# Performance work log

Measured on AMD Instinct MI355X. Metric: run time of the kernel, lower is better.

Reference implementation:

```python
import jax, jax.numpy as jnp
import numpy as np

B, SQ, SKV, D = 4, 4096, 4096, 64

def setup_inputs() -> dict:
    key = jax.random.key(0)
    kq, kv = jax.random.split(key)
    query = jax.random.normal(kq, (B, SQ, D), dtype=jnp.float32)
    value = jax.random.normal(kv, (B, SKV, D), dtype=jnp.float32)
    return {"query": query, "value": value}

def reference(query, value):
    # scores = Q @ V^T  (value acts as both keys and values; no 1/sqrt(d) scaling)
    scores = jnp.einsum('bqd,bkd->bqk', query, value)  # [B, SQ, SKV]
    dist = jax.nn.softmax(scores, axis=-1)
    context = jnp.einsum('bqk,bkd->bqd', dist, value)  # [B, SQ, D]
    return context
```

## Files before the change

kernel.cpp:

```cpp
#include <hip/hip_runtime.h>


#define NB   4
#define SQ   4096
#define SKV  4096
#define DH   64
#define L2E  1.44269504088896340736f

typedef _Float16 half8 __attribute__((ext_vector_type(8)));
typedef _Float16 half4 __attribute__((ext_vector_type(4)));
typedef _Float16 half2v __attribute__((ext_vector_type(2)));
typedef float f32x4 __attribute__((ext_vector_type(4)));
typedef unsigned short u16;

#define MFMA16(a, b, c) __builtin_amdgcn_mfma_f32_16x16x16f16((a), (b), (c), 0, 0, 0)
#define MFMA32(a, b, c) __builtin_amdgcn_mfma_f32_16x16x32_f16((a), (b), (c), 0, 0, 0)

__device__ __forceinline__ u16 f2h(float f) {
  _Float16 h = (_Float16)f;
  return __builtin_bit_cast(u16, h);
}
__device__ __forceinline__ half2v pkrtz(float a, float b) {
  return __builtin_bit_cast(half2v, __builtin_amdgcn_cvt_pkrtz(a, b));
}

__global__ __launch_bounds__(256) void prep_kernel(
    const float* __restrict__ V, u16* __restrict__ vh, u16* __restrict__ vt) {
  __shared__ u16 ldsT[16 * 72];
  int blk = blockIdx.x;
  int b   = blk >> 8;
  int rem = blk & 255;
  int j0  = (rem >> 2) << 6;
  int d0  = (rem & 3) << 4;
  int t   = threadIdx.x;
  int j   = t >> 2;
  int dc  = (t & 3) << 2;

  const float* src = V + ((size_t)(b * SKV) + j0 + j) * DH + d0 + dc;
  float4 v4 = *(const float4*)src;
  u16 h[4] = {f2h(v4.x), f2h(v4.y), f2h(v4.z), f2h(v4.w)};
  unsigned p0 = (unsigned)h[0] | ((unsigned)h[1] << 16);
  unsigned p1 = (unsigned)h[2] | ((unsigned)h[3] << 16);
  size_t go = ((size_t)(b * SKV) + j0 + j) * DH + d0 + dc;
  *(uint2*)(vh + go) = make_uint2(p0, p1);

#pragma unroll
  for (int k = 0; k < 4; ++k) ldsT[(dc + k) * 72 + j] = h[k];
  __syncthreads();

  int dl = t >> 4;
  int jc = (t & 15) << 2;
  u16 tr[4];
#pragma unroll
  for (int k = 0; k < 4; ++k) tr[k] = ldsT[dl * 72 + jc + k];
  unsigned q0 = (unsigned)tr[0] | ((unsigned)tr[1] << 16);
  unsigned q1 = (unsigned)tr[2] | ((unsigned)tr[3] << 16);
  *(uint2*)(vt + ((size_t)(b * DH) + d0 + dl) * SKV + j0 + jc) = make_uint2(q0, q1);
}

__global__ __launch_bounds__(256, 3) void attn_kernel(
    const float* __restrict__ Q,
    const u16* __restrict__ vh,
    const u16* __restrict__ vt,
    u16* __restrict__ po,
    float* __restrict__ pm,
    float* __restrict__ pl,
    int S, int kvLen) {
  __shared__ __align__(16) u16 lds[2][2][64 * 72];

  int blk  = blockIdx.x;
  int tile = blk / S;
  int s    = blk - tile * S;
  int b    = tile >> 5;
  int q0   = (tile & 31) << 7;
  int kv0  = s * kvLen;
  int t    = threadIdx.x;
  int wave = t >> 6;
  int lane = t & 63;
  int col  = lane & 15;
  int quad = lane >> 4;
  int qw   = q0 + (wave << 5);

  half8 qf[2][2];
#pragma unroll
  for (int set = 0; set < 2; ++set) {
#pragma unroll
    for (int kc = 0; kc < 2; ++kc) {
      const float* qp = Q + ((size_t)(b * SQ) + qw + set * 16 + col) * DH +
                        kc * 32 + (quad << 3);
      float4 a0 = *(const float4*)qp;
      float4 a1 = *(const float4*)(qp + 4);
      half8 h;
      h[0] = (_Float16)(a0.x * L2E); h[1] = (_Float16)(a0.y * L2E);
      h[2] = (_Float16)(a0.z * L2E); h[3] = (_Float16)(a0.w * L2E);
      h[4] = (_Float16)(a1.x * L2E); h[5] = (_Float16)(a1.y * L2E);
      h[6] = (_Float16)(a1.z * L2E); h[7] = (_Float16)(a1.w * L2E);
      qf[set][kc] = h;
    }
  }

  f32x4 o[2][4];
  float m_r[2] = {-1e30f, -1e30f};
  float l_r[2] = {0.f, 0.f};
#pragma unroll
  for (int set = 0; set < 2; ++set)
#pragma unroll
    for (int nf = 0; nf < 4; ++nf) o[set][nf] = (f32x4){0.f, 0.f, 0.f, 0.f};

  int sr = t >> 2;
  int sc = (t & 3) << 4;
  const u16* gv  = vh + (size_t)(b * SKV) * DH;
  const u16* gvt = vt + (size_t)(b * DH) * SKV;
  int l0 = sr * 72 + sc;

  {
    size_t g  = (size_t)(kv0 + sr) * DH + sc;
    size_t gt = (size_t)sr * SKV + kv0 + sc;
    *(uint4*)(&lds[0][0][l0])     = *(const uint4*)(gv + g);
    *(uint4*)(&lds[0][0][l0 + 8]) = *(const uint4*)(gv + g + 8);
    *(uint4*)(&lds[0][1][l0])     = *(const uint4*)(gvt + gt);
    *(uint4*)(&lds[0][1][l0 + 8]) = *(const uint4*)(gvt + gt + 8);
  }

  int nIter = kvLen >> 6;
  int cur = 0;
  for (int it = 0; it < nIter; ++it) {
    __syncthreads();

    uint4 a0, a1, c0, c1;
    bool more = (it + 1) < nIter;
    if (more) {
      int j0n = kv0 + ((it + 1) << 6);
      size_t g  = (size_t)(j0n + sr) * DH + sc;
      size_t gt = (size_t)sr * SKV + j0n + sc;
      a0 = *(const uint4*)(gv + g);
      a1 = *(const uint4*)(gv + g + 8);
      c0 = *(const uint4*)(gvt + gt);
      c1 = *(const uint4*)(gvt + gt + 8);
    }

    const u16* sv  = &lds[cur][0][0];
    const u16* svt = &lds[cur][1][0];

    f32x4 sf[2][4];
#pragma unroll
    for (int set = 0; set < 2; ++set)
#pragma unroll
      for (int nf = 0; nf < 4; ++nf) sf[set][nf] = (f32x4){0.f, 0.f, 0.f, 0.f};
#pragma unroll
    for (int nf = 0; nf < 4; ++nf) {
#pragma unroll
      for (int kc = 0; kc < 2; ++kc) {
        half8 av = *(const half8*)(sv + (nf * 16 + col) * 72 + kc * 32 + (quad << 3));
        sf[0][nf] = MFMA32(av, qf[0][kc], sf[0][nf]);
        sf[1][nf] = MFMA32(av, qf[1][kc], sf[1][nf]);
      }
    }

    half4 pf[2][4];
#pragma unroll
    for (int set = 0; set < 2; ++set) {
      float tm = sf[set][0][0];
#pragma unroll
      for (int nf = 0; nf < 4; ++nf)
#pragma unroll
        for (int r = 0; r < 4; ++r) tm = fmaxf(tm, sf[set][nf][r]);
      tm = fmaxf(tm, __shfl_xor(tm, 16, 64));
      tm = fmaxf(tm, __shfl_xor(tm, 32, 64));
      float mn = fmaxf(m_r[set], tm);
      float al = exp2f(m_r[set] - mn);
      m_r[set] = mn;
      float rs = 0.f;
#pragma unroll
      for (int nf = 0; nf < 4; ++nf) {
        float p0 = exp2f(sf[set][nf][0] - mn);
        float p1 = exp2f(sf[set][nf][1] - mn);
        float p2 = exp2f(sf[set][nf][2] - mn);
        float p3 = exp2f(sf[set][nf][3] - mn);
        rs += (p0 + p1) + (p2 + p3);
        half2v lo = pkrtz(p0, p1);
        half2v hi = pkrtz(p2, p3);
        pf[set][nf] = __builtin_shufflevector(lo, hi, 0, 1, 2, 3);
      }
      l_r[set] = l_r[set] * al + rs;
#pragma unroll
      for (int nf = 0; nf < 4; ++nf)
#pragma unroll
        for (int r = 0; r < 4; ++r) o[set][nf][r] *= al;
    }

#pragma unroll
    for (int kc4 = 0; kc4 < 4; ++kc4) {
#pragma unroll
      for (int nf2 = 0; nf2 < 4; ++nf2) {
        half4 avt = *(const half4*)(svt + (nf2 * 16 + col) * 72 + kc4 * 16 + (quad << 2));
        o[0][nf2] = MFMA16(avt, pf[0][kc4], o[0][nf2]);
        o[1][nf2] = MFMA16(avt, pf[1][kc4], o[1][nf2]);
      }
    }

    if (more) {
      u16* dv  = &lds[cur ^ 1][0][0];
      u16* dvt = &lds[cur ^ 1][1][0];
      *(uint4*)(dv + l0)      = a0;
      *(uint4*)(dv + l0 + 8)  = a1;
      *(uint4*)(dvt + l0)     = c0;
      *(uint4*)(dvt + l0 + 8) = c1;
    }
    cur ^= 1;
  }

#pragma unroll
  for (int set = 0; set < 2; ++set) {
    l_r[set] += __shfl_xor(l_r[set], 16, 64);
    l_r[set] += __shfl_xor(l_r[set], 32, 64);
  }
  int pidx = tile * S + s;
  if (quad == 0) {
#pragma unroll
    for (int set = 0; set < 2; ++set) {
      int row = (wave << 5) + set * 16 + col;
      pm[(size_t)pidx * 128 + row] = m_r[set];
      pl[(size_t)pidx * 128 + row] = l_r[set];
    }
  }

  __syncthreads();
  u16* tp = &lds[0][0][0];
#pragma unroll
  for (int set = 0; set < 2; ++set) {
    int q = (wave << 5) + set * 16 + col;
#pragma unroll
    for (int nf2 = 0; nf2 < 4; ++nf2) {
#pragma unroll
      for (int r2 = 0; r2 < 4; r2 += 2) {
        unsigned pk = (unsigned)f2h(o[set][nf2][r2]) |
                      ((unsigned)f2h(o[set][nf2][r2 + 1]) << 16);
        int d = nf2 * 16 + (quad << 2) + r2;
        *(unsigned*)(tp + q * 72 + d) = pk;
      }
    }
  }
  __syncthreads();
  {
    u16* pob = po + (size_t)pidx * 128 * 64;
    int q = t >> 1, hc = (t & 1) << 5;
    uint4 x0 = *(const uint4*)(tp + q * 72 + hc);
    uint4 x1 = *(const uint4*)(tp + q * 72 + hc + 8);
    uint4 x2 = *(const uint4*)(tp + q * 72 + hc + 16);
    uint4 x3 = *(const uint4*)(tp + q * 72 + hc + 24);
    *(uint4*)(pob + q * 64 + hc)      = x0;
    *(uint4*)(pob + q * 64 + hc + 8)  = x1;
    *(uint4*)(pob + q * 64 + hc + 16) = x2;
    *(uint4*)(pob + q * 64 + hc + 24) = x3;
  }
}

__global__ __launch_bounds__(256) void combine_kernel(
    const u16* __restrict__ po,
    const float* __restrict__ pm,
    const float* __restrict__ pl,
    float* __restrict__ out, int S) {
  int t    = threadIdx.x;
  int rowg = blockIdx.x * 32 + (t >> 3);
  int tile = rowg >> 7;
  int row  = rowg & 127;
  int dc   = (t & 7) << 3;

  float mv[8], lv[8];
  float M = -1e30f;
  for (int s = 0; s < S; ++s) {
    mv[s] = pm[(size_t)(tile * S + s) * 128 + row];
    lv[s] = pl[(size_t)(tile * S + s) * 128 + row];
    M = fmaxf(M, mv[s]);
  }
  float L = 0.f, w[8];
  for (int s = 0; s < S; ++s) {
    w[s] = exp2f(mv[s] - M);
    L += lv[s] * w[s];
  }
  float acc[8] = {0.f, 0.f, 0.f, 0.f, 0.f, 0.f, 0.f, 0.f};
  for (int s = 0; s < S; ++s) {
    const u16* p = po + (size_t)(tile * S + s) * 8192 + row * 64 + dc;
    uint4 raw = *(const uint4*)p;
    half8 x = __builtin_bit_cast(half8, raw);
#pragma unroll
    for (int k = 0; k < 8; ++k) acc[k] += w[s] * (float)x[k];
  }
  float invL = 1.0f / L;
  float* op = out + (size_t)rowg * 64 + dc;
  f32x4 o0 = (f32x4){acc[0], acc[1], acc[2], acc[3]};
  f32x4 o1 = (f32x4){acc[4], acc[5], acc[6], acc[7]};
  *(f32x4*)op       = o0 * invL;
  *(f32x4*)(op + 4) = o1 * invL;
}

extern "C" void kernel_launch(void* const* d_in, const int* in_sizes, int n_in,
                              void* d_out, int out_size, void* d_ws, size_t ws_size,
                              hipStream_t stream) {
  const float* Q = (const float*)d_in[0];
  const float* V = (const float*)d_in[1];
  float* out = (float*)d_out;

  const size_t convBytes = (size_t)2 * NB * SKV * DH * 2;
  auto partBytes = [](int S) {
    return (size_t)NB * 32 * S * ((size_t)128 * 64 * 2 + 128 * 8);
  };
  int S = 8;
  while (S > 1 && ws_size < convBytes + partBytes(S)) S >>= 1;
  int kvLen = SKV / S;

  u16* vh = (u16*)d_ws;
  u16* vt = vh + (size_t)NB * SKV * DH;
  u16* po = vt + (size_t)NB * SKV * DH;
  float* pm = (float*)(po + (size_t)NB * 32 * S * 128 * 64);
  float* pl = pm + (size_t)NB * 32 * S * 128;

  prep_kernel<<<NB * 256, 256, 0, stream>>>(V, vh, vt);
  attn_kernel<<<NB * 32 * S, 256, 0, stream>>>(Q, vh, vt, po, pm, pl, S, kvLen);
  combine_kernel<<<NB * SQ / 32, 256, 0, stream>>>(po, pm, pl, out, S);
}
```

Measured before the change: 108.4 us.

## Fuse split-KV combine into attention kernel via last-block atomic counter

Drops the separate combine kernel. Each attention block fences and atomically increments a per-tile counter, and the last block to finish that tile merges the partial outputs, maxes and sums and writes the final result. The counters are zeroed in the prep kernel. This removes one kernel launch and the tail gap between kernels. In exchange, the reduction for each tile runs serially on a single block, and correctness relies on the threadfence and atomic ordering.

```diff
diff --git a/kernel.cpp b/kernel.cpp
--- a/kernel.cpp
+++ b/kernel.cpp
@@ -25,9 +25,11 @@
 }
 
 __global__ __launch_bounds__(256) void prep_kernel(
-    const float* __restrict__ V, u16* __restrict__ vh, u16* __restrict__ vt) {
+    const float* __restrict__ V, u16* __restrict__ vh, u16* __restrict__ vt,
+    unsigned* __restrict__ cnt) {
   __shared__ u16 ldsT[16 * 72];
   int blk = blockIdx.x;
+  if (threadIdx.x == 0 && blk < NB * 32) cnt[blk] = 0;
   int b   = blk >> 8;
   int rem = blk & 255;
   int j0  = (rem >> 2) << 6;
@@ -65,8 +67,11 @@
     u16* __restrict__ po,
     float* __restrict__ pm,
     float* __restrict__ pl,
+    float* __restrict__ out,
+    unsigned* __restrict__ cnt,
     int S, int kvLen) {
   __shared__ __align__(16) u16 lds[2][2][64 * 72];
+  __shared__ unsigned lastFlag;
 
   int blk  = blockIdx.x;
   int tile = blk / S;
@@ -254,45 +259,44 @@
     *(uint4*)(pob + q * 64 + hc + 16) = x2;
     *(uint4*)(pob + q * 64 + hc + 24) = x3;
   }
-}
-
-__global__ __launch_bounds__(256) void combine_kernel(
-    const u16* __restrict__ po,
-    const float* __restrict__ pm,
-    const float* __restrict__ pl,
-    float* __restrict__ out, int S) {
-  int t    = threadIdx.x;
-  int rowg = blockIdx.x * 32 + (t >> 3);
-  int tile = rowg >> 7;
-  int row  = rowg & 127;
-  int dc   = (t & 7) << 3;
-
-  float mv[8], lv[8];
-  float M = -1e30f;
-  for (int s = 0; s < S; ++s) {
-    mv[s] = pm[(size_t)(tile * S + s) * 128 + row];
-    lv[s] = pl[(size_t)(tile * S + s) * 128 + row];
-    M = fmaxf(M, mv[s]);
-  }
-  float L = 0.f, w[8];
-  for (int s = 0; s < S; ++s) {
-    w[s] = exp2f(mv[s] - M);
-    L += lv[s] * w[s];
-  }
-  float acc[8] = {0.f, 0.f, 0.f, 0.f, 0.f, 0.f, 0.f, 0.f};
-  for (int s = 0; s < S; ++s) {
-    const u16* p = po + (size_t)(tile * S + s) * 8192 + row * 64 + dc;
-    uint4 raw = *(const uint4*)p;
-    half8 x = __builtin_bit_cast(half8, raw);
-#pragma unroll
-    for (int k = 0; k < 8; ++k) acc[k] += w[s] * (float)x[k];
-  }
-  float invL = 1.0f / L;
-  float* op = out + (size_t)rowg * 64 + dc;
-  f32x4 o0 = (f32x4){acc[0], acc[1], acc[2], acc[3]};
-  f32x4 o1 = (f32x4){acc[4], acc[5], acc[6], acc[7]};
-  *(f32x4*)op       = o0 * invL;
-  *(f32x4*)(op + 4) = o1 * invL;
+
+  __threadfence();
+  if (t == 0) lastFlag = atomicAdd(&cnt[tile], 1u);
+  __syncthreads();
+  if (lastFlag != (unsigned)(S - 1)) return;
+  __threadfence();
+
+#pragma unroll 1
+  for (int p = 0; p < 4; ++p) {
+    int row = (t >> 3) + (p << 5);
+    int dc  = (t & 7) << 3;
+    float mv[8], lv[8];
+    float M = -1e30f;
+    for (int ss = 0; ss < S; ++ss) {
+      mv[ss] = pm[(size_t)(tile * S + ss) * 128 + row];
+      lv[ss] = pl[(size_t)(tile * S + ss) * 128 + row];
+      M = fmaxf(M, mv[ss]);
+    }
+    float L = 0.f, w[8];
+    for (int ss = 0; ss < S; ++ss) {
+      w[ss] = exp2f(mv[ss] - M);
+      L += lv[ss] * w[ss];
+    }
+    float acc[8] = {0.f, 0.f, 0.f, 0.f, 0.f, 0.f, 0.f, 0.f};
+    for (int ss = 0; ss < S; ++ss) {
+      const u16* pp = po + (size_t)(tile * S + ss) * 8192 + row * 64 + dc;
+      uint4 raw = *(const uint4*)pp;
+      half8 x = __builtin_bit_cast(half8, raw);
+#pragma unroll
+      for (int k = 0; k < 8; ++k) acc[k] += w[ss] * (float)x[k];
+    }
+    float invL = 1.0f / L;
+    float* op = out + ((size_t)tile * 128 + row) * 64 + dc;
+    f32x4 o0 = (f32x4){acc[0], acc[1], acc[2], acc[3]};
+    f32x4 o1 = (f32x4){acc[4], acc[5], acc[6], acc[7]};
+    *(f32x4*)op       = o0 * invL;
+    *(f32x4*)(op + 4) = o1 * invL;
+  }
 }
 
 extern "C" void kernel_launch(void* const* d_in, const int* in_sizes, int n_in,
@@ -304,7 +308,7 @@
 
   const size_t convBytes = (size_t)2 * NB * SKV * DH * 2;
   auto partBytes = [](int S) {
-    return (size_t)NB * 32 * S * ((size_t)128 * 64 * 2 + 128 * 8);
+    return (size_t)NB * 32 * S * ((size_t)128 * 64 * 2 + 128 * 8) + 1024;
   };
   int S = 8;
   while (S > 1 && ws_size < convBytes + partBytes(S)) S >>= 1;
@@ -315,8 +319,9 @@
   u16* po = vt + (size_t)NB * SKV * DH;
   float* pm = (float*)(po + (size_t)NB * 32 * S * 128 * 64);
   float* pl = pm + (size_t)NB * 32 * S * 128;
-
-  prep_kernel<<<NB * 256, 256, 0, stream>>>(V, vh, vt);
-  attn_kernel<<<NB * 32 * S, 256, 0, stream>>>(Q, vh, vt, po, pm, pl, S, kvLen);
-  combine_kernel<<<NB * SQ / 32, 256, 0, stream>>>(po, pm, pl, out, S);
-}
+  unsigned* cnt = (unsigned*)(pl + (size_t)NB * 32 * S * 128);
+
+  prep_kernel<<<NB * 256, 256, 0, stream>>>(V, vh, vt, cnt);
+  attn_kernel<<<NB * 32 * S, 256, 0, stream>>>(Q, vh, vt, po, pm, pl, out, cnt,
+                                               S, kvLen);
+}
```

Result: slower. 350.7 us (+223.7%).
